# Optimization experiments

Hardware: AMD Instinct MI355X
Metric: run time of the kernel (lower is better)

The kernel has to match this reference:

```python
import jax, jax.numpy as jnp
import numpy as np

VOCAB = 50000
PAD_ID = 1
N = 2048
SRC_L = 400


def setup_inputs() -> dict:
    key = jax.random.key(0)
    k1, k2, k3, k4, k5 = jax.random.split(key, 5)
    # probability-like inputs (pointer-generator produces softmax outputs)
    p_gen = jax.nn.softmax(jax.random.normal(k1, (N, VOCAB), dtype=jnp.float32), axis=-1)
    p_copy = jax.nn.softmax(jax.random.normal(k2, (N, SRC_L), dtype=jnp.float32), axis=-1)
    p_switch = jax.random.uniform(k3, (N,), dtype=jnp.float32)
    tgt = jax.random.randint(k4, (N,), 0, VOCAB)
    src = jax.random.randint(k5, (N, SRC_L), 0, VOCAB)
    return {"p_gen": p_gen, "p_copy": p_copy, "p_switch": p_switch, "tgt": tgt, "src": src}


def reference(p_gen, p_copy, p_switch, tgt, src):
    n, vocab = p_gen.shape
    sw = p_switch[:, None]  # [n,1]
    # generation part: p_gen * (1 - p_switch)
    gen_scores = p_gen * (1.0 - sw)
    # copy part: scatter_add p_copy into vocab-sized tensor along src indices
    rows = jnp.arange(n)[:, None]  # [n,1] broadcast with src [n,src_l]
    copy_scores = jnp.zeros((n, vocab), dtype=p_gen.dtype).at[rows, src].add(p_copy)
    # src.max() < vocab_size here, so c_vocab == vocab and the p_switch scale
    # applies to the whole copy distribution (matches torch code in this case)
    scores = copy_scores * sw + gen_scores  # [n, vocab]
    pred = jnp.argmax(scores, axis=1)
    eps = 1e-12
    non_padding = (tgt != PAD_ID).astype(scores.dtype)
    target_scores = jnp.take_along_axis(scores, tgt[:, None], axis=1)[:, 0]
    loss = -jnp.sum(jnp.log(target_scores + eps) * non_padding) / n
    return loss, pred
```

## Files before the change

### kernel.cpp

```cpp
#include <hip/hip_runtime.h>
#include <math.h>

#define NROWS  2048
#define VOCAB  50000
#define NQ     (VOCAB / 4)
#define SRC_L  400
#define PAD_ID 1
#define NBM    1568
#define HSZ    1024
#define QCAP   64
#define PF     4

__global__ __launch_bounds__(256, 8) void pg_row_kernel(
    const float* __restrict__ p_gen,
    const float* __restrict__ p_copy,
    const float* __restrict__ p_switch,
    const int*   __restrict__ tgt,
    const int*   __restrict__ src,
    float* __restrict__ out,
    float* __restrict__ row_loss)
{
    const int row = blockIdx.x;
    const int tid = threadIdx.x;

    const float*  __restrict__ g  = p_gen + (size_t)row * VOCAB;
    const float4* __restrict__ g4 = (const float4*)g;

    __shared__ int      s_src[SRC_L];
    __shared__ float    s_pc [SRC_L];
    __shared__ unsigned s_bm [NBM];
    __shared__ int      s_key[HSZ];
    __shared__ float    s_val[HSZ];
    __shared__ int      s_qs [QCAP];
    __shared__ int      s_qv [QCAP];
    __shared__ int      s_qn;
    __shared__ float    s_gtv;
    __shared__ float    wv[4];
    __shared__ int      wi[4];
    __shared__ float    wsum[4];

    const int  base = row * SRC_L;
    const int  j1ok = (tid + 256 < SRC_L);
    const int   rs0 = src[base + tid];
    const float rp0 = p_copy[base + tid];
    int rs1 = 0; float rp1 = 0.0f;
    if (j1ok) { rs1 = src[base + tid + 256]; rp1 = p_copy[base + tid + 256]; }

    float4 pfv[PF];
    #pragma unroll
    for (int k = 0; k < PF; ++k) pfv[k] = g4[tid + (k << 8)];

    const float sw  = p_switch[row];
    const float osw = 1.0f - sw;
    const int   tv  = tgt[row];

    for (int i = tid; i < NBM; i += 256) s_bm[i] = 0u;
    for (int i = tid; i < HSZ; i += 256) s_key[i] = -1;
    if (tid == 0) s_qn = 0;
    __syncthreads();

    s_src[tid] = rs0; s_pc[tid] = rp0;
    if (j1ok) { s_src[tid + 256] = rs1; s_pc[tid + 256] = rp1; }

    #pragma unroll 2
    for (int rep = 0; rep < 2; ++rep) {
        if (rep == 1 && !j1ok) break;
        const int   v = rep ? rs1 : rs0;
        const float p = rep ? rp1 : rp0;
        atomicOr(&s_bm[v >> 5], 1u << (v & 31));
        unsigned s = (((unsigned)v) * 2654435761u) >> 22;
        while (true) {
            const int old = atomicCAS(&s_key[s], -1, v);
            if (old == -1) { s_val[s] = p; break; }
            if (old == v) {
                const int qi = atomicAdd(&s_qn, 1);
                if (qi < QCAP) { s_qs[qi] = (int)s; s_qv[qi] = v; }
                break;
            }
            s = (s + 1) & (HSZ - 1);
        }
    }
    __syncthreads();

    if (tid < 64) {
        int qn = s_qn; if (qn > QCAP) qn = QCAP;
        const int lane = tid;
        for (int q = 0; q < qn; ++q) {
            const int slot = s_qs[q];
            const int v    = s_qv[q];
            float S = 0.0f;
            #pragma unroll
            for (int r = 0; r < 7; ++r) {
                const int k  = (r << 6) + lane;
                const int kk = (k < SRC_L) ? k : 0;
                const bool m = (k < SRC_L) && (s_src[kk] == v);
                const float pk = s_pc[kk];
                unsigned long long mask = __ballot(m);
                while (mask) {
                    const int l = __ffsll((long long)mask) - 1;
                    S = __fadd_rn(S, __shfl(pk, l));
                    mask &= mask - 1;
                }
            }
            if (lane == 0) s_val[slot] = S;
        }
    }
    __syncthreads();

    float bestv = -1.0f;
    int   besti = 0x7fffffff;

    #define PG_ELT(b, i, comp)                                                  \
    {                                                                           \
        const float a = __fmul_rn(comp, osw);                                   \
        if (a > bestv) { bestv = a; besti = (b) + (i); }                        \
        if (m4 & (1u << (i))) {                                                 \
            const int v = (b) + (i);                                            \
            unsigned hs = (((unsigned)v) * 2654435761u) >> 22;                  \
            while (s_key[hs] != v) hs = (hs + 1) & (HSZ - 1);                   \
            const float cand = __fadd_rn(__fmul_rn(sw, s_val[hs]),              \
                                         __fmul_rn(osw, comp));                 \
            if (cand > bestv) { bestv = cand; besti = v; }                      \
        }                                                                       \
    }

    #define PG_QUAD(t, vv)                                                      \
    {                                                                           \
        const int b = (t) << 2;                                                 \
        const unsigned m4 = (s_bm[b >> 5] >> (b & 31)) & 0xFu;                  \
        PG_ELT(b, 0, (vv).x)                                                    \
        PG_ELT(b, 1, (vv).y)                                                    \
        PG_ELT(b, 2, (vv).z)                                                    \
        PG_ELT(b, 3, (vv).w)                                                    \
        if (tv >= b && tv < b + 4) {                                            \
            float gt = (vv).x;                                                  \
            if      (tv == b + 1) gt = (vv).y;                                  \
            else if (tv == b + 2) gt = (vv).z;                                  \
            else if (tv == b + 3) gt = (vv).w;                                  \
            s_gtv = gt;                                                         \
        }                                                                       \
    }

    #pragma unroll
    for (int k = 0; k < PF; ++k) { const int t = tid + (k << 8); PG_QUAD(t, pfv[k]) }

    int t = tid + (PF << 8);
    for (; t + 256 < NQ; t += 512) {
        const float4 va = g4[t];
        const float4 vb = g4[t + 256];
        PG_QUAD(t, va)
        PG_QUAD(t + 256, vb)
    }
    if (t < NQ) {
        const float4 vc = g4[t];
        PG_QUAD(t, vc)
    }
    #undef PG_QUAD
    #undef PG_ELT

    float tsum = 0.0f;
    for (int k = tid; k < SRC_L; k += 256)
        if (s_src[k] == tv) tsum += s_pc[k];

    for (int off = 32; off > 0; off >>= 1) {
        const float ov = __shfl_down(bestv, off);
        const int   oi = __shfl_down(besti, off);
        if (ov > bestv || (ov == bestv && oi < besti)) { bestv = ov; besti = oi; }
        tsum += __shfl_down(tsum, off);
    }

    const int wave = tid >> 6;
    if ((tid & 63) == 0) { wv[wave] = bestv; wi[wave] = besti; wsum[wave] = tsum; }
    __syncthreads();

    if (tid == 0) {
        for (int w = 1; w < 4; ++w) {
            if (wv[w] > bestv || (wv[w] == bestv && wi[w] < besti)) {
                bestv = wv[w]; besti = wi[w];
            }
            tsum += wsum[w];
        }
        out[1 + row] = (float)besti;

        const float ts = __fadd_rn(__fmul_rn(sw, tsum), __fmul_rn(osw, s_gtv));
        row_loss[row] = (tv != PAD_ID) ? logf(ts + 1e-12f) : 0.0f;
    }
}

__global__ __launch_bounds__(256) void pg_loss_kernel(
    const float* __restrict__ row_loss,
    float* __restrict__ out)
{
    float s = 0.0f;
    for (int i = threadIdx.x; i < NROWS; i += 256) s += row_loss[i];
    for (int off = 32; off > 0; off >>= 1) s += __shfl_down(s, off);

    __shared__ float wsum[4];
    if ((threadIdx.x & 63) == 0) wsum[threadIdx.x >> 6] = s;
    __syncthreads();
    if (threadIdx.x == 0) {
        const float t = wsum[0] + wsum[1] + wsum[2] + wsum[3];
        out[0] = -t / (float)NROWS;
    }
}

extern "C" void kernel_launch(void* const* d_in, const int* in_sizes, int n_in,
                              void* d_out, int out_size, void* d_ws, size_t ws_size,
                              hipStream_t stream) {
    const float* p_gen    = (const float*)d_in[0];
    const float* p_copy   = (const float*)d_in[1];
    const float* p_switch = (const float*)d_in[2];
    const int*   tgt      = (const int*)d_in[3];
    const int*   src      = (const int*)d_in[4];

    float* out      = (float*)d_out;
    float* row_loss = (float*)d_ws;

    pg_row_kernel<<<NROWS, 256, 0, stream>>>(p_gen, p_copy, p_switch, tgt, src,
                                             out, row_loss);
    pg_loss_kernel<<<1, 256, 0, stream>>>(row_loss, out);
}
```

Measured before the change: 83.41 us.

## Stream vocab argmax before building copy hash, then rescore copied tokens

Moves the full p_gen streaming pass, which handles only the generation term, ahead of the shared-memory hash construction. The bitmap and its per-element probes go away. After the hash is built, each occupied slot re-reads p_gen at that token and scores the combined copy+gen value, with a tie-break on the lower index. This drops the bitmap init and atomics, and lets the global-memory stream start without waiting on the hash-build barriers, at the cost of about 400 scattered re-reads per row. It also lowers shared memory per block.

```diff
diff --git a/kernel.cpp b/kernel.cpp
--- a/kernel.cpp
+++ b/kernel.cpp
@@ -6,7 +6,6 @@
 #define NQ     (VOCAB / 4)
 #define SRC_L  400
 #define PAD_ID 1
-#define NBM    1568
 #define HSZ    1024
 #define QCAP   64
 #define PF     4
@@ -28,7 +27,6 @@
 
     __shared__ int      s_src[SRC_L];
     __shared__ float    s_pc [SRC_L];
-    __shared__ unsigned s_bm [NBM];
     __shared__ int      s_key[HSZ];
     __shared__ float    s_val[HSZ];
     __shared__ int      s_qs [QCAP];
@@ -54,20 +52,58 @@
     const float osw = 1.0f - sw;
     const int   tv  = tgt[row];
 
-    for (int i = tid; i < NBM; i += 256) s_bm[i] = 0u;
     for (int i = tid; i < HSZ; i += 256) s_key[i] = -1;
     if (tid == 0) s_qn = 0;
-    __syncthreads();
+
+    float bestv = -1.0f;
+    int   besti = 0x7fffffff;
+
+    #define PG_QUAD(t, vv)                                                      \
+    {                                                                           \
+        const int b = (t) << 2;                                                 \
+        float a;                                                                \
+        a = __fmul_rn((vv).x, osw);                                             \
+        if (a > bestv) { bestv = a; besti = b;     }                            \
+        a = __fmul_rn((vv).y, osw);                                             \
+        if (a > bestv) { bestv = a; besti = b + 1; }                            \
+        a = __fmul_rn((vv).z, osw);                                             \
+        if (a > bestv) { bestv = a; besti = b + 2; }                            \
+        a = __fmul_rn((vv).w, osw);                                             \
+        if (a > bestv) { bestv = a; besti = b + 3; }                            \
+        if (tv >= b && tv < b + 4) {                                            \
+            float gt = (vv).x;                                                  \
+            if      (tv == b + 1) gt = (vv).y;                                  \
+            else if (tv == b + 2) gt = (vv).z;                                  \
+            else if (tv == b + 3) gt = (vv).w;                                  \
+            s_gtv = gt;                                                         \
+        }                                                                       \
+    }
+
+    #pragma unroll
+    for (int k = 0; k < PF; ++k) { const int t = tid + (k << 8); PG_QUAD(t, pfv[k]) }
+
+    int t = tid + (PF << 8);
+    for (; t + 256 < NQ; t += 512) {
+        const float4 va = g4[t];
+        const float4 vb = g4[t + 256];
+        PG_QUAD(t, va)
+        PG_QUAD(t + 256, vb)
+    }
+    if (t < NQ) {
+        const float4 vc = g4[t];
+        PG_QUAD(t, vc)
+    }
+    #undef PG_QUAD
 
     s_src[tid] = rs0; s_pc[tid] = rp0;
     if (j1ok) { s_src[tid + 256] = rs1; s_pc[tid + 256] = rp1; }
+    __syncthreads();
 
     #pragma unroll 2
     for (int rep = 0; rep < 2; ++rep) {
         if (rep == 1 && !j1ok) break;
         const int   v = rep ? rs1 : rs0;
         const float p = rep ? rp1 : rp0;
-        atomicOr(&s_bm[v >> 5], 1u << (v & 31));
         unsigned s = (((unsigned)v) * 2654435761u) >> 22;
         while (true) {
             const int old = atomicCAS(&s_key[s], -1, v);
@@ -107,56 +143,17 @@
     }
     __syncthreads();
 
-    float bestv = -1.0f;
-    int   besti = 0x7fffffff;
-
-    #define PG_ELT(b, i, comp)                                                  \
-    {                                                                           \
-        const float a = __fmul_rn(comp, osw);                                   \
-        if (a > bestv) { bestv = a; besti = (b) + (i); }                        \
-        if (m4 & (1u << (i))) {                                                 \
-            const int v = (b) + (i);                                            \
-            unsigned hs = (((unsigned)v) * 2654435761u) >> 22;                  \
-            while (s_key[hs] != v) hs = (hs + 1) & (HSZ - 1);                   \
-            const float cand = __fadd_rn(__fmul_rn(sw, s_val[hs]),              \
-                                         __fmul_rn(osw, comp));                 \
-            if (cand > bestv) { bestv = cand; besti = v; }                      \
-        }                                                                       \
-    }
-
-    #define PG_QUAD(t, vv)                                                      \
-    {                                                                           \
-        const int b = (t) << 2;                                                 \
-        const unsigned m4 = (s_bm[b >> 5] >> (b & 31)) & 0xFu;                  \
-        PG_ELT(b, 0, (vv).x)                                                    \
-        PG_ELT(b, 1, (vv).y)                                                    \
-        PG_ELT(b, 2, (vv).z)                                                    \
-        PG_ELT(b, 3, (vv).w)                                                    \
-        if (tv >= b && tv < b + 4) {                                            \
-            float gt = (vv).x;                                                  \
-            if      (tv == b + 1) gt = (vv).y;                                  \
-            else if (tv == b + 2) gt = (vv).z;                                  \
-            else if (tv == b + 3) gt = (vv).w;                                  \
-            s_gtv = gt;                                                         \
-        }                                                                       \
-    }
-
-    #pragma unroll
-    for (int k = 0; k < PF; ++k) { const int t = tid + (k << 8); PG_QUAD(t, pfv[k]) }
-
-    int t = tid + (PF << 8);
-    for (; t + 256 < NQ; t += 512) {
-        const float4 va = g4[t];
-        const float4 vb = g4[t + 256];
-        PG_QUAD(t, va)
-        PG_QUAD(t + 256, vb)
-    }
-    if (t < NQ) {
-        const float4 vc = g4[t];
-        PG_QUAD(t, vc)
-    }
-    #undef PG_QUAD
-    #undef PG_ELT
+    for (int s = tid; s < HSZ; s += 256) {
+        const int v = s_key[s];
+        if (v >= 0) {
+            const float gv   = g[v];
+            const float cand = __fadd_rn(__fmul_rn(sw, s_val[s]),
+                                         __fmul_rn(osw, gv));
+            if (cand > bestv || (cand == bestv && v < besti)) {
+                bestv = cand; besti = v;
+            }
+        }
+    }
 
     float tsum = 0.0f;
     for (int k = tid; k < SRC_L; k += 256)
```

Result: slower. 86.83 us (+4.1%).

## Split each row's vocab scan across two blocks and merge argmax in final kernel

Applied to the files above, without the earlier changes.

Each row is now handled by two blocks, each scanning half the vocabulary with its own half-size bitmap and hash table, and only inserting source tokens that fall in its half. Per-half argmax results go to workspace, and the final kernel combines them and sums the loss. This doubles the grid to 4096 blocks and shrinks per-block work to improve load balance and tail effects. In exchange, both blocks still load all of src and p_copy and build a table, the final kernel does more serial work, and sw*osw data is duplicated.

```diff
diff --git a/kernel.cpp b/kernel.cpp
--- a/kernel.cpp
+++ b/kernel.cpp
@@ -3,32 +3,37 @@
 
 #define NROWS  2048
 #define VOCAB  50000
-#define NQ     (VOCAB / 4)
+#define HALF_V 25000
+#define NQH    (HALF_V / 4)
 #define SRC_L  400
 #define PAD_ID 1
-#define NBM    1568
-#define HSZ    1024
+#define NBMH   784
+#define HSZ    512
 #define QCAP   64
 #define PF     4
 
-__global__ __launch_bounds__(256, 8) void pg_row_kernel(
+__global__ __launch_bounds__(256, 8) void pg_half_kernel(
     const float* __restrict__ p_gen,
     const float* __restrict__ p_copy,
     const float* __restrict__ p_switch,
     const int*   __restrict__ tgt,
     const int*   __restrict__ src,
-    float* __restrict__ out,
+    float* __restrict__ half_bv,
+    int*   __restrict__ half_bi,
     float* __restrict__ row_loss)
 {
-    const int row = blockIdx.x;
-    const int tid = threadIdx.x;
-
-    const float*  __restrict__ g  = p_gen + (size_t)row * VOCAB;
+    const int bid  = blockIdx.x;
+    const int row  = bid >> 1;
+    const int half = bid & 1;
+    const int lo   = half * HALF_V;
+    const int tid  = threadIdx.x;
+
+    const float*  __restrict__ g  = p_gen + (size_t)row * VOCAB + lo;
     const float4* __restrict__ g4 = (const float4*)g;
 
     __shared__ int      s_src[SRC_L];
     __shared__ float    s_pc [SRC_L];
-    __shared__ unsigned s_bm [NBM];
+    __shared__ unsigned s_bm [NBMH];
     __shared__ int      s_key[HSZ];
     __shared__ float    s_val[HSZ];
     __shared__ int      s_qs [QCAP];
@@ -50,34 +55,39 @@
     #pragma unroll
     for (int k = 0; k < PF; ++k) pfv[k] = g4[tid + (k << 8)];
 
-    const float sw  = p_switch[row];
-    const float osw = 1.0f - sw;
-    const int   tv  = tgt[row];
-
-    for (int i = tid; i < NBM; i += 256) s_bm[i] = 0u;
-    for (int i = tid; i < HSZ; i += 256) s_key[i] = -1;
+    const float sw   = p_switch[row];
+    const float osw  = 1.0f - sw;
+    const int   tv   = tgt[row];
+    const int   tvl  = tv - lo;
+    const bool  own  = ((unsigned)tvl < (unsigned)HALF_V);
+
+    for (int i = tid; i < NBMH; i += 256) s_bm[i] = 0u;
+    for (int i = tid; i < HSZ;  i += 256) s_key[i] = -1;
     if (tid == 0) s_qn = 0;
-    __syncthreads();
 
     s_src[tid] = rs0; s_pc[tid] = rp0;
     if (j1ok) { s_src[tid + 256] = rs1; s_pc[tid + 256] = rp1; }
+    __syncthreads();
 
     #pragma unroll 2
     for (int rep = 0; rep < 2; ++rep) {
         if (rep == 1 && !j1ok) break;
         const int   v = rep ? rs1 : rs0;
         const float p = rep ? rp1 : rp0;
-        atomicOr(&s_bm[v >> 5], 1u << (v & 31));
-        unsigned s = (((unsigned)v) * 2654435761u) >> 22;
-        while (true) {
-            const int old = atomicCAS(&s_key[s], -1, v);
-            if (old == -1) { s_val[s] = p; break; }
-            if (old == v) {
-                const int qi = atomicAdd(&s_qn, 1);
-                if (qi < QCAP) { s_qs[qi] = (int)s; s_qv[qi] = v; }
-                break;
+        const int  vl = v - lo;
+        if ((unsigned)vl < (unsigned)HALF_V) {
+            atomicOr(&s_bm[vl >> 5], 1u << (vl & 31));
+            unsigned s = (((unsigned)v) * 2654435761u) >> 23;
+            while (true) {
+                const int old = atomicCAS(&s_key[s], -1, v);
+                if (old == -1) { s_val[s] = p; break; }
+                if (old == v) {
+                    const int qi = atomicAdd(&s_qn, 1);
+                    if (qi < QCAP) { s_qs[qi] = (int)s; s_qv[qi] = v; }
+                    break;
+                }
+                s = (s + 1) & (HSZ - 1);
             }
-            s = (s + 1) & (HSZ - 1);
         }
     }
     __syncthreads();
@@ -113,10 +123,10 @@
     #define PG_ELT(b, i, comp)                                                  \
     {                                                                           \
         const float a = __fmul_rn(comp, osw);                                   \
-        if (a > bestv) { bestv = a; besti = (b) + (i); }                        \
+        if (a > bestv) { bestv = a; besti = lo + (b) + (i); }                   \
         if (m4 & (1u << (i))) {                                                 \
-            const int v = (b) + (i);                                            \
-            unsigned hs = (((unsigned)v) * 2654435761u) >> 22;                  \
+            const int v = lo + (b) + (i);                                       \
+            unsigned hs = (((unsigned)v) * 2654435761u) >> 23;                  \
             while (s_key[hs] != v) hs = (hs + 1) & (HSZ - 1);                   \
             const float cand = __fadd_rn(__fmul_rn(sw, s_val[hs]),              \
                                          __fmul_rn(osw, comp));                 \
@@ -132,11 +142,11 @@
         PG_ELT(b, 1, (vv).y)                                                    \
         PG_ELT(b, 2, (vv).z)                                                    \
         PG_ELT(b, 3, (vv).w)                                                    \
-        if (tv >= b && tv < b + 4) {                                            \
+        if (own && tvl >= b && tvl < b + 4) {                                   \
             float gt = (vv).x;                                                  \
-            if      (tv == b + 1) gt = (vv).y;                                  \
-            else if (tv == b + 2) gt = (vv).z;                                  \
-            else if (tv == b + 3) gt = (vv).w;                                  \
+            if      (tvl == b + 1) gt = (vv).y;                                 \
+            else if (tvl == b + 2) gt = (vv).z;                                 \
+            else if (tvl == b + 3) gt = (vv).w;                                 \
             s_gtv = gt;                                                         \
         }                                                                       \
     }
@@ -145,13 +155,13 @@
     for (int k = 0; k < PF; ++k) { const int t = tid + (k << 8); PG_QUAD(t, pfv[k]) }
 
     int t = tid + (PF << 8);
-    for (; t + 256 < NQ; t += 512) {
+    for (; t + 256 < NQH; t += 512) {
         const float4 va = g4[t];
         const float4 vb = g4[t + 256];
         PG_QUAD(t, va)
         PG_QUAD(t + 256, vb)
     }
-    if (t < NQ) {
+    if (t < NQH) {
         const float4 vc = g4[t];
         PG_QUAD(t, vc)
     }
@@ -180,19 +190,29 @@
             }
             tsum += wsum[w];
         }
-        out[1 + row] = (float)besti;
-
-        const float ts = __fadd_rn(__fmul_rn(sw, tsum), __fmul_rn(osw, s_gtv));
-        row_loss[row] = (tv != PAD_ID) ? logf(ts + 1e-12f) : 0.0f;
+        half_bv[bid] = bestv;
+        half_bi[bid] = besti;
+
+        if (own) {
+            const float ts = __fadd_rn(__fmul_rn(sw, tsum), __fmul_rn(osw, s_gtv));
+            row_loss[row] = (tv != PAD_ID) ? logf(ts + 1e-12f) : 0.0f;
+        }
     }
 }
 
-__global__ __launch_bounds__(256) void pg_loss_kernel(
+__global__ __launch_bounds__(256) void pg_final_kernel(
+    const float* __restrict__ half_bv,
+    const int*   __restrict__ half_bi,
     const float* __restrict__ row_loss,
     float* __restrict__ out)
 {
     float s = 0.0f;
-    for (int i = threadIdx.x; i < NROWS; i += 256) s += row_loss[i];
+    for (int r = threadIdx.x; r < NROWS; r += 256) {
+        const float bv0 = half_bv[2 * r], bv1 = half_bv[2 * r + 1];
+        const int   bi0 = half_bi[2 * r], bi1 = half_bi[2 * r + 1];
+        out[1 + r] = (float)((bv1 > bv0) ? bi1 : bi0);
+        s += row_loss[r];
+    }
     for (int off = 32; off > 0; off >>= 1) s += __shfl_down(s, off);
 
     __shared__ float wsum[4];
@@ -214,9 +234,11 @@
     const int*   src      = (const int*)d_in[4];
 
     float* out      = (float*)d_out;
-    float* row_loss = (float*)d_ws;
-
-    pg_row_kernel<<<NROWS, 256, 0, stream>>>(p_gen, p_copy, p_switch, tgt, src,
-                                             out, row_loss);
-    pg_loss_kernel<<<1, 256, 0, stream>>>(row_loss, out);
+    float* half_bv  = (float*)d_ws;
+    int*   half_bi  = (int*)((char*)d_ws + 4096 * sizeof(float));
+    float* row_loss = (float*)((char*)d_ws + 8192 * sizeof(float));
+
+    pg_half_kernel<<<2 * NROWS, 256, 0, stream>>>(p_gen, p_copy, p_switch, tgt,
+                                                  src, half_bv, half_bi, row_loss);
+    pg_final_kernel<<<1, 256, 0, stream>>>(half_bv, half_bi, row_loss, out);
 }
```

Result: no change. 83.64 us (+0.3%).
